# Optimization experiments

Hardware: AMD Instinct MI355X
Metric: run time of the kernel (lower is better)

## Reference

```python
import jax, jax.numpy as jnp
import numpy as np

SCALE = 64.0
MARGIN = 0.5
COS_M = float(np.cos(MARGIN))
SIN_M = float(np.sin(MARGIN))
TH = float(np.cos(np.pi - MARGIN))
MM = float(np.sin(np.pi - MARGIN) * MARGIN)
B, D, C = 1024, 512, 50000


def setup_inputs() -> dict:
    key = jax.random.key(0)
    k1, k2, k3 = jax.random.split(key, 3)
    embeddings = jax.random.normal(k1, (B, D), dtype=jnp.float32)
    labels = jax.random.randint(k2, (B,), 0, C, dtype=jnp.int32)
    # xavier_uniform over (num_classes, embedding_dim)
    limit = float(np.sqrt(6.0 / (C + D)))
    weight = jax.random.uniform(k3, (C, D), dtype=jnp.float32, minval=-limit, maxval=limit)
    return {"embeddings": embeddings, "labels": labels, "weight": weight}


def _l2norm(x, axis=-1, eps=1e-12):
    # matches F.normalize(p=2): x / max(||x||, eps)
    n = jnp.sqrt(jnp.sum(x * x, axis=axis, keepdims=True))
    return x / jnp.maximum(n, eps)


def reference(embeddings, labels, weight):
    e = _l2norm(embeddings, axis=1)          # [B, D]
    w = _l2norm(weight, axis=1)              # [C, D]
    cosine = jnp.einsum('bd,cd->bc', e, w)   # [B, C]
    sine = jnp.sqrt(1.0 - jnp.clip(cosine * cosine, 0.0, 1.0))
    phi = cosine * COS_M - sine * SIN_M
    phi = jnp.where(cosine > TH, phi, cosine - MM)
    one_hot = jax.nn.one_hot(labels, cosine.shape[1], dtype=cosine.dtype)
    logits = SCALE * (one_hot * phi + (1.0 - one_hot) * cosine)
    # cross_entropy with integer labels, mean reduction
    logp = jax.nn.log_softmax(logits, axis=1)
    nll = -jnp.take_along_axis(logp, labels[:, None].astype(jnp.int32), axis=1)[:, 0]
    return jnp.mean(nll)
```

## Files before the change

kernel.cpp:

```cpp
#include <hip/hip_runtime.h>
#include <hip/hip_bf16.h>
#include <cstdint>

#define BB 1024
#define DD 512
#define CC 50000
#define CCP 50048
#define NTN 782
#define NBLK 512
#define SCALE_F 64.0f
#define COS_M_F 0.87758256189037276f
#define SIN_M_F 0.47942553860420301f
#define TH_F   (-0.87758256189037276f)
#define MM_F   0.23971276930210156f

typedef __attribute__((ext_vector_type(4))) int i32x4;
typedef __attribute__((ext_vector_type(8))) char char8;

#define OFF_RS   ((size_t)0)
#define OFF_ES   (OFF_RS + 4096)
#define OFF_WS   (OFF_ES + 4096)
#define OFF_EI8  (OFF_WS + 204800)
#define OFF_WI8  (OFF_EI8 + (size_t)BB*DD)

__global__ void quant_kernel(const float* __restrict__ emb, const float* __restrict__ wgt,
                             char* __restrict__ ei8, float* __restrict__ es,
                             char* __restrict__ wi8, float* __restrict__ wsc,
                             float* __restrict__ rowsum, float* __restrict__ out) {
    const int blk = blockIdx.x;
    if (blk == 12756) {
        const int t = threadIdx.x;
        #pragma unroll
        for (int i = 0; i < 4; ++i) rowsum[i * 256 + t] = 0.f;
        if (t == 0) out[0] = 0.f;
        int4* pz = reinterpret_cast<int4*>(wi8 + (size_t)CC * DD + t * 96);
        #pragma unroll
        for (int i = 0; i < 6; ++i) pz[i] = (int4){0, 0, 0, 0};
        if (t < CCP - CC) wsc[CC + t] = 0.f;
        return;
    }
    const int r4 = threadIdx.x >> 6;
    const int l  = threadIdx.x & 63;
    const bool isw = blk < 12500;
    const int row = isw ? (blk * 4 + r4) : ((blk - 12500) * 4 + r4);
    const float* src = (isw ? wgt : emb) + (size_t)row * DD;
    const float4* r = reinterpret_cast<const float4*>(src);
    float4 v0 = r[l * 2 + 0];
    float4 v1 = r[l * 2 + 1];
    float ss = v0.x*v0.x + v0.y*v0.y + v0.z*v0.z + v0.w*v0.w
             + v1.x*v1.x + v1.y*v1.y + v1.z*v1.z + v1.w*v1.w;
    float mx = fmaxf(fmaxf(fmaxf(fabsf(v0.x), fabsf(v0.y)), fmaxf(fabsf(v0.z), fabsf(v0.w))),
                     fmaxf(fmaxf(fabsf(v1.x), fabsf(v1.y)), fmaxf(fabsf(v1.z), fabsf(v1.w))));
    #pragma unroll
    for (int m = 1; m < 64; m <<= 1) {
        ss += __shfl_xor(ss, m);
        mx = fmaxf(mx, __shfl_xor(mx, m));
    }
    float nrm = fmaxf(sqrtf(ss), 1e-12f);
    float ma  = fmaxf(mx, 1e-20f);
    float qs  = 127.0f / ma;
    if (l == 0) (isw ? wsc : es)[row] = ma / (127.0f * nrm);
    char8 q;
    q[0]=(char)__float2int_rn(v0.x*qs); q[1]=(char)__float2int_rn(v0.y*qs);
    q[2]=(char)__float2int_rn(v0.z*qs); q[3]=(char)__float2int_rn(v0.w*qs);
    q[4]=(char)__float2int_rn(v1.x*qs); q[5]=(char)__float2int_rn(v1.y*qs);
    q[6]=(char)__float2int_rn(v1.z*qs); q[7]=(char)__float2int_rn(v1.w*qs);
    *reinterpret_cast<char8*>((isw ? wi8 : ei8) + (size_t)row * DD + l * 8) = q;
}

__global__ __launch_bounds__(512, 4) void arc_gemm_i8_kernel(
        const char* __restrict__ ei8,
        const char* __restrict__ wi8,
        const float* __restrict__ es,
        const float* __restrict__ wsc,
        float* __restrict__ rowsum)
{
    __shared__ __align__(16) char lds[2][32768];

    const int t   = threadIdx.x;
    const int wid = t >> 6;
    const int wm  = wid >> 1;
    const int wn  = wid & 1;
    const int l   = t & 63;
    const int r16 = l & 15;
    const int kg  = l >> 4;

    const int bid  = blockIdx.x;
    const int bidp = (bid & 7) * 64 + (bid >> 3);
    const int mt = bidp & 7;
    const int s  = bidp >> 3;
    const int m0 = mt * 128;
    const int nt0 = (s < 14) ? s * 13 : 12 * s + 14;
    const int cnt = (s < 14) ? 13 : 12;

    i32x4 af[2][8];
    #pragma unroll
    for (int fm = 0; fm < 2; ++fm)
        #pragma unroll
        for (int kk = 0; kk < 8; ++kk)
            af[fm][kk] = *reinterpret_cast<const i32x4*>(
                ei8 + (size_t)(m0 + wm * 32 + fm * 16 + r16) * DD + kk * 64 + kg * 16);

    float se_r[2][4];
    #pragma unroll
    for (int fm = 0; fm < 2; ++fm)
        #pragma unroll
        for (int j = 0; j < 4; ++j)
            se_r[fm][j] = es[m0 + wm * 32 + fm * 16 + kg * 4 + j];

    float rs[2][4];
    #pragma unroll
    for (int fm = 0; fm < 2; ++fm)
        #pragma unroll
        for (int j = 0; j < 4; ++j) rs[fm][j] = 0.f;

    const char* sp[4];
    #pragma unroll
    for (int i = 0; i < 4; ++i) {
        int flat = (i * 512 + t) * 16;
        int kk2  = flat >> 13;
        int row  = (flat >> 7) & 63;
        int col  = flat & 127;
        int scol = col ^ ((row & 7) << 4);
        sp[i] = wi8 + (size_t)(nt0 * 64 + row) * DD + kk2 * 128 + scol;
    }
    auto stageB = [&](int buf) {
        #pragma unroll
        for (int i = 0; i < 4; ++i) {
            __builtin_amdgcn_global_load_lds(
                (const __attribute__((address_space(1))) void*)sp[i],
                (__attribute__((address_space(3))) void*)(&lds[buf][(i * 512 + t) * 16]),
                16, 0, 0);
            sp[i] += 64 * DD;
        }
    };
    const float* wp = wsc + nt0 * 64 + wn * 32 + r16;

    stageB(0);
    asm volatile("s_waitcnt vmcnt(0)" ::: "memory");
    __builtin_amdgcn_s_barrier();

    for (int i = 0; i < cnt; ++i) {
        const int buf = i & 1;
        if (i + 1 < cnt) stageB(buf ^ 1);

        float sw64_0 = wp[0]  * SCALE_F;
        float sw64_1 = wp[16] * SCALE_F;
        wp += 64;

        i32x4 acc[2][2];
        #pragma unroll
        for (int fm = 0; fm < 2; ++fm)
            #pragma unroll
            for (int fn = 0; fn < 2; ++fn) acc[fm][fn] = (i32x4){0, 0, 0, 0};
        #pragma unroll
        for (int kk = 0; kk < 8; ++kk) {
            i32x4 b[2];
            #pragma unroll
            for (int fn = 0; fn < 2; ++fn) {
                int row = wn * 32 + fn * 16 + r16;
                int off = (kk >> 1) * 8192 + row * 128
                        + (((kk & 1) * 64 + kg * 16) ^ ((row & 7) << 4));
                b[fn] = *reinterpret_cast<const i32x4*>(&lds[buf][off]);
            }
            #pragma unroll
            for (int fm = 0; fm < 2; ++fm)
                #pragma unroll
                for (int fn = 0; fn < 2; ++fn)
                    acc[fm][fn] = __builtin_amdgcn_mfma_i32_16x16x64_i8(af[fm][kk], b[fn], acc[fm][fn], 0, 0, 0);
        }

        #pragma unroll
        for (int fm = 0; fm < 2; ++fm)
            #pragma unroll
            for (int j = 0; j < 4; ++j) {
                float k0 = se_r[fm][j] * sw64_0;
                float k1 = se_r[fm][j] * sw64_1;
                rs[fm][j] += __expf(fmaf((float)acc[fm][0][j], k0, -SCALE_F));
                rs[fm][j] += __expf(fmaf((float)acc[fm][1][j], k1, -SCALE_F));
            }

        asm volatile("s_waitcnt vmcnt(0)" ::: "memory");
        __builtin_amdgcn_s_barrier();
    }

    #pragma unroll
    for (int fm = 0; fm < 2; ++fm) {
        #pragma unroll
        for (int j = 0; j < 4; ++j) {
            float v = rs[fm][j];
            #pragma unroll
            for (int mk = 1; mk < 16; mk <<= 1) v += __shfl_xor(v, mk);
            if (r16 == 0) {
                int grow = m0 + wm * 32 + fm * 16 + kg * 4 + j;
                atomicAdd(&rowsum[grow], v);
            }
        }
    }
}

__global__ void finish_kernel(const char* __restrict__ ei8, const char* __restrict__ wi8,
                              const float* __restrict__ es, const float* __restrict__ wsc,
                              const int* __restrict__ labels,
                              const float* __restrict__ rowsum, float* __restrict__ out) {
    const int b = blockIdx.x;
    const int l = threadIdx.x;
    const int lab = labels[b];
    char8 a = *reinterpret_cast<const char8*>(ei8 + (size_t)b * DD + l * 8);
    char8 w = *reinterpret_cast<const char8*>(wi8 + (size_t)lab * DD + l * 8);
    int d = 0;
    #pragma unroll
    for (int k = 0; k < 8; ++k) d += (int)a[k] * (int)w[k];
    #pragma unroll
    for (int m = 1; m < 64; m <<= 1) d += __shfl_xor(d, m);
    if (l == 0) {
        float kf  = es[b] * (wsc[lab] * SCALE_F);
        float sub = __expf(fmaf((float)d, kf, -SCALE_F));
        float cosv = (float)d * es[b] * wsc[lab];
        float c2 = fminf(fmaxf(cosv * cosv, 0.f), 1.f);
        float phi = cosv * COS_M_F - sqrtf(1.f - c2) * SIN_M_F;
        phi = (cosv > TH_F) ? phi : (cosv - MM_F);
        float ml = SCALE_F * phi;
        float Sf = rowsum[b] + __expf(ml - SCALE_F) - sub;
        float nll = -(ml - SCALE_F - logf(Sf));
        atomicAdd(out, nll * (1.0f / BB));
    }
}

extern "C" void kernel_launch(void* const* d_in, const int* in_sizes, int n_in,
                              void* d_out, int out_size, void* d_ws, size_t ws_size,
                              hipStream_t stream) {
    const float* emb    = (const float*)d_in[0];
    const int*   labels = (const int*)d_in[1];
    const float* wgt    = (const float*)d_in[2];
    float* out = (float*)d_out;
    char* ws = (char*)d_ws;

    float* rowsum = (float*)(ws + OFF_RS);
    float* es     = (float*)(ws + OFF_ES);
    float* wsc    = (float*)(ws + OFF_WS);
    char*  ei8    = (char*)(ws + OFF_EI8);
    char*  wi8    = (char*)(ws + OFF_WI8);

    quant_kernel<<<12757, 256, 0, stream>>>(emb, wgt, ei8, es, wi8, wsc, rowsum, out);
    arc_gemm_i8_kernel<<<NBLK, 512, 0, stream>>>(ei8, wi8, es, wsc, rowsum);
    finish_kernel<<<BB, 64, 0, stream>>>(ei8, wi8, es, wsc, labels, rowsum, out);
}
```

Measured before the change: 76.46 us.

## Triple-buffer weight tiles, halve grid, and preload weight scales into LDS

```diff
diff --git a/kernel.cpp b/kernel.cpp
--- a/kernel.cpp
+++ b/kernel.cpp
@@ -7,7 +7,7 @@
 #define CC 50000
 #define CCP 50048
 #define NTN 782
-#define NBLK 512
+#define NBLK 256
 #define SCALE_F 64.0f
 #define COS_M_F 0.87758256189037276f
 #define SIN_M_F 0.47942553860420301f
@@ -68,14 +68,15 @@
     *reinterpret_cast<char8*>((isw ? wi8 : ei8) + (size_t)row * DD + l * 8) = q;
 }
 
-__global__ __launch_bounds__(512, 4) void arc_gemm_i8_kernel(
+__global__ __launch_bounds__(512, 2) void arc_gemm_i8_kernel(
         const char* __restrict__ ei8,
         const char* __restrict__ wi8,
         const float* __restrict__ es,
         const float* __restrict__ wsc,
         float* __restrict__ rowsum)
 {
-    __shared__ __align__(16) char lds[2][32768];
+    __shared__ __align__(16) char lds[3][32768];
+    __shared__ float ldsW[1600];
 
     const int t   = threadIdx.x;
     const int wid = t >> 6;
@@ -86,12 +87,12 @@
     const int kg  = l >> 4;
 
     const int bid  = blockIdx.x;
-    const int bidp = (bid & 7) * 64 + (bid >> 3);
+    const int bidp = (bid & 7) * 32 + (bid >> 3);
     const int mt = bidp & 7;
-    const int s  = bidp >> 3;
+    const int sp = bidp >> 3;
     const int m0 = mt * 128;
-    const int nt0 = (s < 14) ? s * 13 : 12 * s + 14;
-    const int cnt = (s < 14) ? 13 : 12;
+    const int nt0 = (sp < 14) ? sp * 25 : sp * 24 + 14;
+    const int cnt = (sp < 14) ? 25 : 24;
 
     i32x4 af[2][8];
     #pragma unroll
@@ -114,7 +115,10 @@
         #pragma unroll
         for (int j = 0; j < 4; ++j) rs[fm][j] = 0.f;
 
-    const char* sp[4];
+    for (int j = t; j < cnt * 64; j += 512)
+        ldsW[j] = wsc[nt0 * 64 + j];
+
+    const char* sp4[4];
     #pragma unroll
     for (int i = 0; i < 4; ++i) {
         int flat = (i * 512 + t) * 16;
@@ -122,31 +126,28 @@
         int row  = (flat >> 7) & 63;
         int col  = flat & 127;
         int scol = col ^ ((row & 7) << 4);
-        sp[i] = wi8 + (size_t)(nt0 * 64 + row) * DD + kk2 * 128 + scol;
+        sp4[i] = wi8 + (size_t)(nt0 * 64 + row) * DD + kk2 * 128 + scol;
     }
     auto stageB = [&](int buf) {
         #pragma unroll
         for (int i = 0; i < 4; ++i) {
             __builtin_amdgcn_global_load_lds(
-                (const __attribute__((address_space(1))) void*)sp[i],
+                (const __attribute__((address_space(1))) void*)sp4[i],
                 (__attribute__((address_space(3))) void*)(&lds[buf][(i * 512 + t) * 16]),
                 16, 0, 0);
-            sp[i] += 64 * DD;
+            sp4[i] += 64 * DD;
         }
     };
-    const float* wp = wsc + nt0 * 64 + wn * 32 + r16;
 
     stageB(0);
-    asm volatile("s_waitcnt vmcnt(0)" ::: "memory");
+    stageB(1);
+    asm volatile("s_waitcnt vmcnt(4)" ::: "memory");
     __builtin_amdgcn_s_barrier();
 
+    int cur = 0;
     for (int i = 0; i < cnt; ++i) {
-        const int buf = i & 1;
-        if (i + 1 < cnt) stageB(buf ^ 1);
-
-        float sw64_0 = wp[0]  * SCALE_F;
-        float sw64_1 = wp[16] * SCALE_F;
-        wp += 64;
+        int stg = cur + 2; if (stg >= 3) stg -= 3;
+        if (i + 2 < cnt) stageB(stg);
 
         i32x4 acc[2][2];
         #pragma unroll
@@ -161,7 +162,7 @@
                 int row = wn * 32 + fn * 16 + r16;
                 int off = (kk >> 1) * 8192 + row * 128
                         + (((kk & 1) * 64 + kg * 16) ^ ((row & 7) << 4));
-                b[fn] = *reinterpret_cast<const i32x4*>(&lds[buf][off]);
+                b[fn] = *reinterpret_cast<const i32x4*>(&lds[cur][off]);
             }
             #pragma unroll
             for (int fm = 0; fm < 2; ++fm)
@@ -170,6 +171,8 @@
                     acc[fm][fn] = __builtin_amdgcn_mfma_i32_16x16x64_i8(af[fm][kk], b[fn], acc[fm][fn], 0, 0, 0);
         }
 
+        float sw64_0 = ldsW[i * 64 + wn * 32 + r16]      * SCALE_F;
+        float sw64_1 = ldsW[i * 64 + wn * 32 + r16 + 16] * SCALE_F;
         #pragma unroll
         for (int fm = 0; fm < 2; ++fm)
             #pragma unroll
@@ -180,8 +183,10 @@
                 rs[fm][j] += __expf(fmaf((float)acc[fm][1][j], k1, -SCALE_F));
             }
 
-        asm volatile("s_waitcnt vmcnt(0)" ::: "memory");
+        if (i + 2 < cnt)      { asm volatile("s_waitcnt vmcnt(4)" ::: "memory"); }
+        else if (i + 1 < cnt) { asm volatile("s_waitcnt vmcnt(0)" ::: "memory"); }
         __builtin_amdgcn_s_barrier();
+        cur += 1; if (cur >= 3) cur -= 3;
     }
 
     #pragma unroll
```

New measurement: 80.12 us. +4.8%, slower.
